# Kernel optimization log

Measured on AMD Instinct MI355X. Metric: run time of the kernel, lower is better.

Reference implementation:

```python
import jax, jax.numpy as jnp
import numpy as np

NUM_CLASSES = 100000
FEAT_DIM = 128
BATCH = 1024


def setup_inputs() -> dict:
    key = jax.random.key(0)
    k1, k2, k3 = jax.random.split(key, 3)
    x = jax.random.normal(k1, (BATCH, FEAT_DIM), dtype=jnp.float32)
    labels = jax.random.randint(k2, (BATCH,), 0, NUM_CLASSES, dtype=jnp.int64)
    centers = jax.random.normal(k3, (NUM_CLASSES, FEAT_DIM), dtype=jnp.float32)
    return {"x": x, "labels": labels, "centers": centers}


def reference(x, labels, centers):
    # Faithful to the torch module: full [B, C] pairwise squared-distance
    # matrix, label mask, clamp, sum / B.  Note the original clamps the
    # MASKED matrix, so every off-label zero is clamped up to 1e-12 and
    # contributes to the sum; we replicate that exactly.
    B = x.shape[0]
    C = centers.shape[0]
    x_sq = jnp.sum(x * x, axis=1, keepdims=True)            # [B, 1]
    c_sq = jnp.sum(centers * centers, axis=1)[None, :]       # [1, C]
    distmat = x_sq + c_sq - 2.0 * (x @ centers.T)            # [B, C]
    mask = (labels[:, None] == jnp.arange(C, dtype=labels.dtype)[None, :])
    dist = distmat * mask.astype(distmat.dtype)
    dist = jnp.clip(dist, 1e-12, 1e12)
    return jnp.sum(dist) / B
```

## Files before the change

kernel.cpp:

```cpp
#include <hip/hip_runtime.h>


#define CL_B 1024
#define CL_D 128
#define CL_C 100000

__global__ __launch_bounds__(64) void cl_per_sample(
    const float* __restrict__ x,
    const int* __restrict__ labels,
    const float* __restrict__ centers,
    float* __restrict__ ws) {
    const int b = blockIdx.x;
    const int t = threadIdx.x;
    const int lab = labels[b];

    const float2* xp = reinterpret_cast<const float2*>(x + (size_t)b * CL_D);
    const float2* cp = reinterpret_cast<const float2*>(centers + (size_t)lab * CL_D);
    const float2 xv = xp[t];
    const float2 cv = cp[t];
    const float d0 = xv.x - cv.x;
    const float d1 = xv.y - cv.y;
    float s = d0 * d0 + d1 * d1;

    #pragma unroll
    for (int off = 32; off > 0; off >>= 1)
        s += __shfl_down(s, off, 64);

    if (t == 0) {
        s = fminf(fmaxf(s, 1e-12f), 1e12f);
        ws[b] = s;
    }
}

__global__ __launch_bounds__(256) void cl_reduce(
    const float* __restrict__ ws,
    float* __restrict__ out) {
    const int t = threadIdx.x;
    float s = 0.0f;
    #pragma unroll
    for (int i = 0; i < CL_B / 256; ++i)
        s += ws[t + i * 256];

    #pragma unroll
    for (int off = 32; off > 0; off >>= 1)
        s += __shfl_down(s, off, 64);

    __shared__ float sm[4];
    if ((t & 63) == 0) sm[t >> 6] = s;
    __syncthreads();
    if (t == 0) {
        const float tot = sm[0] + sm[1] + sm[2] + sm[3];
        out[0] = tot / (float)CL_B + (float)(CL_C - 1) * 1e-12f;
    }
}

extern "C" void kernel_launch(void* const* d_in, const int* in_sizes, int n_in,
                              void* d_out, int out_size, void* d_ws, size_t ws_size,
                              hipStream_t stream) {
    const float* x       = (const float*)d_in[0];
    const int*   labels  = (const int*)d_in[1];
    const float* centers = (const float*)d_in[2];
    float* out = (float*)d_out;
    float* ws  = (float*)d_ws;

    cl_per_sample<<<CL_B, 64, 0, stream>>>(x, labels, centers, ws);
    cl_reduce<<<1, 256, 0, stream>>>(ws, out);
}
```

Measured before the change: 10.81 us.

## Fuse per-sample and reduce kernels into one launch with last-block reduction

```diff
diff --git a/kernel.cpp b/kernel.cpp
--- a/kernel.cpp
+++ b/kernel.cpp
@@ -4,53 +4,61 @@
 #define CL_B 1024
 #define CL_D 128
 #define CL_C 100000
+#define NBLK 64
+#define SPB  (CL_B / NBLK)
+#define SPW  (SPB / 4)
 
-__global__ __launch_bounds__(64) void cl_per_sample(
+__global__ __launch_bounds__(256) void cl_onekernel(
     const float* __restrict__ x,
     const int* __restrict__ labels,
     const float* __restrict__ centers,
-    float* __restrict__ ws) {
-    const int b = blockIdx.x;
-    const int t = threadIdx.x;
-    const int lab = labels[b];
+    float* __restrict__ partials,
+    unsigned int* __restrict__ counter,
+    float* __restrict__ out) {
+    const int t    = threadIdx.x;
+    const int wave = t >> 6;
+    const int lane = t & 63;
 
-    const float2* xp = reinterpret_cast<const float2*>(x + (size_t)b * CL_D);
-    const float2* cp = reinterpret_cast<const float2*>(centers + (size_t)lab * CL_D);
-    const float2 xv = xp[t];
-    const float2 cv = cp[t];
-    const float d0 = xv.x - cv.x;
-    const float d1 = xv.y - cv.y;
-    float s = d0 * d0 + d1 * d1;
+    float acc = 0.0f;
+    const int base = blockIdx.x * SPB + wave * SPW;
+    #pragma unroll
+    for (int i = 0; i < SPW; ++i) {
+        const int b   = base + i;
+        const int lab = labels[b];
+        const float2 xv = reinterpret_cast<const float2*>(x + (size_t)b * CL_D)[lane];
+        const float2 cv = reinterpret_cast<const float2*>(centers + (size_t)lab * CL_D)[lane];
+        const float d0 = xv.x - cv.x;
+        const float d1 = xv.y - cv.y;
+        float s = d0 * d0 + d1 * d1;
+        #pragma unroll
+        for (int off = 32; off > 0; off >>= 1)
+            s += __shfl_down(s, off, 64);
+        if (lane == 0)
+            acc += fminf(fmaxf(s, 1e-12f), 1e12f);
+    }
 
-    #pragma unroll
-    for (int off = 32; off > 0; off >>= 1)
-        s += __shfl_down(s, off, 64);
+    __shared__ float sm[4];
+    __shared__ int   is_last;
+    if (lane == 0) sm[wave] = acc;
+    __syncthreads();
 
     if (t == 0) {
-        s = fminf(fmaxf(s, 1e-12f), 1e12f);
-        ws[b] = s;
+        partials[blockIdx.x] = sm[0] + sm[1] + sm[2] + sm[3];
+        __threadfence();
+        const unsigned old = atomicAdd(counter, 1u);
+        is_last = (old == NBLK - 1u);
+        if (is_last) __threadfence();
     }
-}
+    __syncthreads();
 
-__global__ __launch_bounds__(256) void cl_reduce(
-    const float* __restrict__ ws,
-    float* __restrict__ out) {
-    const int t = threadIdx.x;
-    float s = 0.0f;
-    #pragma unroll
-    for (int i = 0; i < CL_B / 256; ++i)
-        s += ws[t + i * 256];
-
-    #pragma unroll
-    for (int off = 32; off > 0; off >>= 1)
-        s += __shfl_down(s, off, 64);
-
-    __shared__ float sm[4];
-    if ((t & 63) == 0) sm[t >> 6] = s;
-    __syncthreads();
-    if (t == 0) {
-        const float tot = sm[0] + sm[1] + sm[2] + sm[3];
-        out[0] = tot / (float)CL_B + (float)(CL_C - 1) * 1e-12f;
+    if (is_last && wave == 0) {
+        volatile const float* vp = partials;
+        float v = vp[lane];
+        #pragma unroll
+        for (int off = 32; off > 0; off >>= 1)
+            v += __shfl_down(v, off, 64);
+        if (lane == 0)
+            out[0] = v / (float)CL_B + (float)(CL_C - 1) * 1e-12f;
     }
 }
 
@@ -61,8 +69,9 @@
     const int*   labels  = (const int*)d_in[1];
     const float* centers = (const float*)d_in[2];
     float* out = (float*)d_out;
-    float* ws  = (float*)d_ws;
+    float* partials = (float*)d_ws;
+    unsigned int* counter = (unsigned int*)((char*)d_ws + NBLK * sizeof(float));
 
-    cl_per_sample<<<CL_B, 64, 0, stream>>>(x, labels, centers, ws);
-    cl_reduce<<<1, 256, 0, stream>>>(ws, out);
+    hipMemsetAsync(counter, 0, sizeof(unsigned int), stream);
+    cl_onekernel<<<NBLK, 256, 0, stream>>>(x, labels, centers, partials, counter, out);
 }
```

New measurement: 14.24 us. 1.32x slower.
